# Performance work log

Hardware: AMD Instinct MI355X
Metric: run time of the kernel (lower is better)

The kernel has to match this reference:

```python
import jax, jax.numpy as jnp
import numpy as np

NUM_HEADS = 8
IN_DIM = 384
HEAD_DIM = IN_DIM // NUM_HEADS  # 48


def setup_inputs() -> dict:
    key = jax.random.key(0)
    ks = jax.random.split(key, 6)
    B, N, M, C = 4, 4096, 1024, 384
    q_x = jax.random.normal(ks[0], (B, N, C), dtype=jnp.float32)
    kv_x = jax.random.normal(ks[1], (B, M, C), dtype=jnp.float32)
    s = C ** -0.5  # fan-in style init scale
    Wq = jax.random.normal(ks[2], (C, IN_DIM), dtype=jnp.float32) * s
    Wkv = jax.random.normal(ks[3], (C, 2 * IN_DIM), dtype=jnp.float32) * s
    Wproj = jax.random.normal(ks[4], (IN_DIM, IN_DIM), dtype=jnp.float32) * (IN_DIM ** -0.5)
    bproj = jnp.zeros((IN_DIM,), dtype=jnp.float32)
    return {"q_x": q_x, "kv_x": kv_x, "Wq": Wq, "Wkv": Wkv, "Wproj": Wproj, "bproj": bproj}


def reference(q_x, kv_x, Wq, Wkv, Wproj, bproj):
    B, N, C = q_x.shape
    M = kv_x.shape[1]
    scale = HEAD_DIM ** -0.5
    # q: [B, H, N, hd]
    q = (q_x @ Wq).reshape(B, N, NUM_HEADS, HEAD_DIM).transpose(0, 2, 1, 3)
    # k, v: [B, H, M, hd]
    kv = (kv_x @ Wkv).reshape(B, M, 2, NUM_HEADS, HEAD_DIM).transpose(2, 0, 3, 1, 4)
    k, v = kv[0], kv[1]
    # attention scores [B, H, N, M]
    attn = jax.nn.softmax(jnp.einsum('bhnd,bhmd->bhnm', q, k) * scale, axis=-1)
    x = jnp.einsum('bhnm,bhmd->bhnd', attn, v)  # [B, H, N, hd]
    x = x.transpose(0, 2, 1, 3).reshape(B, N, IN_DIM)
    x = x @ Wproj + bproj
    # sr_ratio == 1 residual: add raw q projection back
    q_res = q.transpose(0, 2, 1, 3).reshape(B, N, IN_DIM)
    return q_res + x
```

## Files before the change

### kernel.cpp

```cpp
#include <hip/hip_runtime.h>
#include <hip/hip_bf16.h>
#include <math.h>

#define B_ 4
#define N_ 4096
#define M_ 1024
#define C_ 384
#define NH_ 8
#define HD_ 48

typedef float f32x4 __attribute__((ext_vector_type(4)));
typedef float f32x16 __attribute__((ext_vector_type(16)));
typedef short bf16x8 __attribute__((ext_vector_type(8)));

typedef __attribute__((address_space(3))) unsigned int lds_uint;
typedef const __attribute__((address_space(1))) unsigned int glob_uint;

__device__ __forceinline__ void gld_lds16(const void* g, void* l) {
    __builtin_amdgcn_global_load_lds((glob_uint*)g, (lds_uint*)l, 16, 0, 0);
}

__device__ __forceinline__ unsigned short f2bf(float x) {
    unsigned int u = __builtin_bit_cast(unsigned int, x);
    return (unsigned short)((u + 0x7FFFu + ((u >> 16) & 1u)) >> 16);
}
__device__ __forceinline__ float bf2f(unsigned short x) {
    return __builtin_bit_cast(float, (unsigned int)x << 16);
}
__device__ __forceinline__ float fast_exp2(float x) {
#if __has_builtin(__builtin_amdgcn_exp2f)
    return __builtin_amdgcn_exp2f(x);
#else
    return exp2f(x);
#endif
}
__device__ __forceinline__ uint2 pack4_rne(float a, float b, float c, float d) {
    uint2 r;
    r.x = (unsigned int)f2bf(a) | ((unsigned int)f2bf(b) << 16);
    r.y = (unsigned int)f2bf(c) | ((unsigned int)f2bf(d) << 16);
    return r;
}

#define QSCALE 0.20823490983597203f
#define INV_QSCALE (1.0f / 0.20823490983597203f)

__global__ __launch_bounds__(256)
void prep(const float* __restrict__ qx_f, unsigned short* __restrict__ qx_bf,
          const float* __restrict__ kvx_f, unsigned short* __restrict__ kvx_bf,
          const float* __restrict__ Wq, const float* __restrict__ Wkv,
          const float* __restrict__ Wproj,
          unsigned short* __restrict__ Wq_t, unsigned short* __restrict__ Wkv_t,
          unsigned short* __restrict__ Wproj_t)
{
    __shared__ unsigned short T[64 * 72];
    const int tid = threadIdx.x;
    int bid = blockIdx.x;

    if (bid < 7680) {
        size_t i4 = (size_t)bid * 256 + tid;
        const float* src; unsigned short* dst;
        if (i4 < 1572864u) { src = qx_f; dst = qx_bf; }
        else { src = kvx_f; dst = kvx_bf; i4 -= 1572864u; }
        float4 v = *(const float4*)&src[i4 * 4];
        *(uint2*)&dst[i4 * 4] = pack4_rne(v.x, v.y, v.z, v.w);
        return;
    }

    bid -= 7680;
    const float* W; unsigned short* Wt; int N, kt, nt;
    if (bid < 36)       { W = Wq;    Wt = Wq_t;    N = 384; kt = bid / 6;  nt = bid - kt * 6; }
    else if (bid < 108) { bid -= 36;  W = Wkv;   Wt = Wkv_t;   N = 768; kt = bid / 12; nt = bid - kt * 12; }
    else                { bid -= 108; W = Wproj; Wt = Wproj_t; N = 384; kt = bid / 6;  nt = bid - kt * 6; }
    const int k0 = kt * 64, n0 = nt * 64;

    #pragma unroll
    for (int it = 0; it < 4; ++it) {
        int k = it * 16 + (tid >> 4);
        int n4 = (tid & 15) * 4;
        float4 v = *(const float4*)&W[(size_t)(k0 + k) * N + n0 + n4];
        T[(n4 + 0) * 72 + k] = f2bf(v.x);
        T[(n4 + 1) * 72 + k] = f2bf(v.y);
        T[(n4 + 2) * 72 + k] = f2bf(v.z);
        T[(n4 + 3) * 72 + k] = f2bf(v.w);
    }
    __syncthreads();
    #pragma unroll
    for (int i = 0; i < 2; ++i) {
        int s = tid + 256 * i;
        int n = s >> 3, part = s & 7;
        *(uint4*)&Wt[(size_t)(n0 + n) * C_ + k0 + part * 8] = *(const uint4*)&T[n * 72 + part * 8];
    }
}

__device__ __forceinline__ void stage128(const unsigned short* src, unsigned short* lds,
                                         int kk, int tid) {
    #pragma unroll
    for (int r = 0; r < 4; ++r) {
        int off = r * 256 + tid;
        int row = off >> 3;
        int c = off & 7;
        int gc = c ^ (row & 7);
        gld_lds16(src + (size_t)row * C_ + kk + gc * 8, lds + (size_t)off * 8);
    }
}
__device__ __forceinline__ void stage64(const unsigned short* src, unsigned short* lds,
                                        int kk, int tid) {
    #pragma unroll
    for (int r = 0; r < 2; ++r) {
        int off = r * 256 + tid;
        int row = off >> 3;
        int c = off & 7;
        int gc = c ^ (row & 7);
        gld_lds16(src + (size_t)row * C_ + kk + gc * 8, lds + (size_t)off * 8);
    }
}
__device__ __forceinline__ bf16x8 frag_ld(const unsigned short* lds, int row, int chunk) {
    return *(const bf16x8*)&lds[row * 64 + ((chunk ^ (row & 7)) << 3)];
}

#define GEMM_CORE(Aptr, Wptr)                                                        \
    f32x4 acc[4][4];                                                                 \
    _Pragma("unroll")                                                                \
    for (int rt = 0; rt < 4; ++rt)                                                   \
        _Pragma("unroll")                                                            \
        for (int ct = 0; ct < 4; ++ct) acc[rt][ct] = (f32x4){0.f, 0.f, 0.f, 0.f};    \
    const int wrow0 = (wave & 1) * 64;                                               \
    const int wcol0 = (wave >> 1) * 64;                                              \
    for (int kk = 0; kk < C_; kk += 64) {                                            \
        __syncthreads();                                                             \
        stage128(Aptr, As, kk, tid);                                                 \
        stage128(Wptr, Ws, kk, tid);                                                 \
        __syncthreads();                                                             \
        _Pragma("unroll")                                                            \
        for (int ks = 0; ks < 2; ++ks) {                                             \
            bf16x8 af[4], wf[4];                                                     \
            _Pragma("unroll")                                                        \
            for (int rt = 0; rt < 4; ++rt)                                           \
                af[rt] = frag_ld(As, wrow0 + rt * 16 + ln, ks * 4 + quad);           \
            _Pragma("unroll")                                                        \
            for (int ct = 0; ct < 4; ++ct)                                           \
                wf[ct] = frag_ld(Ws, wcol0 + ct * 16 + ln, ks * 4 + quad);           \
            _Pragma("unroll")                                                        \
            for (int rt = 0; rt < 4; ++rt)                                           \
                _Pragma("unroll")                                                    \
                for (int ct = 0; ct < 4; ++ct)                                       \
                    acc[rt][ct] = __builtin_amdgcn_mfma_f32_16x16x32_bf16(           \
                        wf[ct], af[rt], acc[rt][ct], 0, 0, 0);                       \
        }                                                                            \
    }

__global__ __launch_bounds__(256)
void gemm_qkv(const unsigned short* __restrict__ qx, const unsigned short* __restrict__ kvx,
              const unsigned short* __restrict__ Wqt, const unsigned short* __restrict__ Wkvt,
              unsigned short* __restrict__ qbf,
              unsigned short* __restrict__ kbf, unsigned short* __restrict__ vbf)
{
    __shared__ unsigned short As[128 * 64];
    __shared__ unsigned short Ws[128 * 64];
    const int tid = threadIdx.x;
    const int wave = tid >> 6;
    const int lane = tid & 63;
    const int ln = lane & 15;
    const int quad = lane >> 4;

    int bid = blockIdx.x;
    int mode, row0, col0;
    const unsigned short *A, *Wt;
    if (bid < 384) { mode = 0; A = qx;  Wt = Wqt;  row0 = (bid / 3) * 128; col0 = (bid % 3) * 128; }
    else { bid -= 384; mode = 1; A = kvx; Wt = Wkvt; row0 = (bid / 6) * 128; col0 = (bid % 6) * 128; }

    GEMM_CORE(A + (size_t)row0 * C_, Wt + (size_t)col0 * C_)

    #pragma unroll
    for (int rt = 0; rt < 4; ++rt) {
        int grow = row0 + wrow0 + rt * 16 + ln;
        #pragma unroll
        for (int ct = 0; ct < 4; ++ct) {
            int col = col0 + wcol0 + ct * 16 + quad * 4;
            f32x4 v = acc[rt][ct];
            if (mode == 0) {
                int b = grow >> 12, n = grow & (N_ - 1);
                int h = col / HD_, d = col - h * HD_;
                *(uint2*)&qbf[(((size_t)(b * NH_ + h) * N_) + n) * HD_ + d] =
                    pack4_rne(v[0] * QSCALE, v[1] * QSCALE, v[2] * QSCALE, v[3] * QSCALE);
            } else {
                int b = grow >> 10, m = grow & (M_ - 1);
                if (col < C_) {
                    int h = col / HD_, d = col - h * HD_;
                    *(uint2*)&kbf[(((size_t)(b * NH_ + h) * M_) + m) * HD_ + d] =
                        pack4_rne(v[0], v[1], v[2], v[3]);
                } else {
                    int c2 = col - C_;
                    int h = c2 / HD_, d = c2 - h * HD_;
                    size_t base = ((size_t)(b * NH_ + h) * HD_ + d) * M_ + m;
                    #pragma unroll
                    for (int r = 0; r < 4; ++r) vbf[base + (size_t)r * M_] = f2bf(v[r]);
                }
            }
        }
    }
}

__global__ __launch_bounds__(256)
void gemm_out(const unsigned short* __restrict__ A, const unsigned short* __restrict__ Wt,
              float* __restrict__ out0,
              const unsigned short* __restrict__ qbf, const float* __restrict__ bias)
{
    __shared__ unsigned short As[128 * 64];
    __shared__ unsigned short Ws[64 * 64];
    const int tid = threadIdx.x;
    const int wave = tid >> 6;
    const int lane = tid & 63;
    const int ln = lane & 15;
    const int quad = lane >> 4;
    const int row0 = (blockIdx.x / 6) * 128;
    const int col0 = (blockIdx.x % 6) * 64;
    const int wrow0 = (wave & 1) * 64;
    const int wcol0 = (wave >> 1) * 32;

    f32x4 acc[4][2];
    #pragma unroll
    for (int rt = 0; rt < 4; ++rt)
        #pragma unroll
        for (int ct = 0; ct < 2; ++ct) acc[rt][ct] = (f32x4){0.f, 0.f, 0.f, 0.f};

    const unsigned short* Ap = A + (size_t)row0 * C_;
    const unsigned short* Wp = Wt + (size_t)col0 * C_;
    for (int kk = 0; kk < C_; kk += 64) {
        __syncthreads();
        stage128(Ap, As, kk, tid);
        stage64(Wp, Ws, kk, tid);
        __syncthreads();
        #pragma unroll
        for (int ks = 0; ks < 2; ++ks) {
            bf16x8 af[4], wf[2];
            #pragma unroll
            for (int rt = 0; rt < 4; ++rt)
                af[rt] = frag_ld(As, wrow0 + rt * 16 + ln, ks * 4 + quad);
            #pragma unroll
            for (int ct = 0; ct < 2; ++ct)
                wf[ct] = frag_ld(Ws, wcol0 + ct * 16 + ln, ks * 4 + quad);
            #pragma unroll
            for (int rt = 0; rt < 4; ++rt)
                #pragma unroll
                for (int ct = 0; ct < 2; ++ct)
                    acc[rt][ct] = __builtin_amdgcn_mfma_f32_16x16x32_bf16(
                        wf[ct], af[rt], acc[rt][ct], 0, 0, 0);
        }
    }

    #pragma unroll
    for (int rt = 0; rt < 4; ++rt) {
        int grow = row0 + wrow0 + rt * 16 + ln;
        #pragma unroll
        for (int ct = 0; ct < 2; ++ct) {
            int col = col0 + wcol0 + ct * 16 + quad * 4;
            f32x4 v = acc[rt][ct];
            size_t idx = (size_t)grow * C_ + col;
            int b = grow >> 12, n = grow & (N_ - 1);
            int h = col / HD_, d = col - h * HD_;
            uint2 ad = *(const uint2*)&qbf[(((size_t)(b * NH_ + h) * N_) + n) * HD_ + d];
            float4 bi = *(const float4*)&bias[col];
            float4 o;
            o.x = v[0] + bf2f((unsigned short)(ad.x & 0xFFFF)) * INV_QSCALE + bi.x;
            o.y = v[1] + bf2f((unsigned short)(ad.x >> 16))    * INV_QSCALE + bi.y;
            o.z = v[2] + bf2f((unsigned short)(ad.y & 0xFFFF)) * INV_QSCALE + bi.z;
            o.w = v[3] + bf2f((unsigned short)(ad.y >> 16))    * INV_QSCALE + bi.w;
            *(float4*)&out0[idx] = o;
        }
    }
}

__device__ __forceinline__ void attn_load(bf16x8 (&ka)[3], bf16x8 (&va)[2][2],
                                          const unsigned short* kb,
                                          const unsigned short* vb,
                                          int m0, int l31, int hi)
{
    #pragma unroll
    for (int s = 0; s < 3; ++s)
        ka[s] = *(const bf16x8*)&kb[(size_t)(m0 + l31) * HD_ + s * 16 + hi * 8];
    #pragma unroll
    for (int ot2 = 0; ot2 < 2; ++ot2)
        #pragma unroll
        for (int s2 = 0; s2 < 2; ++s2)
            va[ot2][s2] = *(const bf16x8*)&vb[(size_t)(ot2 * 32 + l31) * M_ + m0 + s2 * 16 + hi * 8];
}

__device__ __forceinline__ void attn_compute(const bf16x8 (&ka)[3], const bf16x8 (&va)[2][2],
                                             const bf16x8 (&qb)[2][3],
                                             f32x16 (&O)[2][2], float (&rs)[2], int hi)
{
    #pragma unroll
    for (int qt = 0; qt < 2; ++qt) {
        f32x16 S;
        #pragma unroll
        for (int r = 0; r < 16; ++r) S[r] = 0.f;
        __builtin_amdgcn_s_setprio(1);
        #pragma unroll
        for (int s = 0; s < 3; ++s)
            S = __builtin_amdgcn_mfma_f32_32x32x16_bf16(ka[s], qb[qt][s], S, 0, 0, 0);
        __builtin_amdgcn_s_setprio(0);

        float p[16];
        #pragma unroll
        for (int r = 0; r < 16; ++r) p[r] = fast_exp2(S[r]);
        {
            float s0 = (p[0] + p[1]) + (p[2] + p[3]);
            float s1 = (p[4] + p[5]) + (p[6] + p[7]);
            float s2 = (p[8] + p[9]) + (p[10] + p[11]);
            float s3 = (p[12] + p[13]) + (p[14] + p[15]);
            rs[qt] += (s0 + s1) + (s2 + s3);
        }

        unsigned c0[4], c1[4];
        #pragma unroll
        for (int g = 0; g < 4; ++g) {
            c0[g] = (__builtin_bit_cast(unsigned int, p[4 * g + 0]) >> 16) |
                    (__builtin_bit_cast(unsigned int, p[4 * g + 1]) & 0xFFFF0000u);
            c1[g] = (__builtin_bit_cast(unsigned int, p[4 * g + 2]) >> 16) |
                    (__builtin_bit_cast(unsigned int, p[4 * g + 3]) & 0xFFFF0000u);
        }

        #pragma unroll
        for (int s2 = 0; s2 < 2; ++s2) {
            unsigned o00 = c0[2 * s2], o01 = c0[2 * s2 + 1];
            unsigned o10 = c1[2 * s2], o11 = c1[2 * s2 + 1];
            unsigned pr0 = (unsigned)__shfl_xor((int)(hi ? o00 : o01), 32);
            unsigned pr1 = (unsigned)__shfl_xor((int)(hi ? o10 : o11), 32);
            unsigned d0 = hi ? pr0 : o00;
            unsigned d1 = hi ? pr1 : o10;
            unsigned d2 = hi ? o01 : pr0;
            unsigned d3 = hi ? o11 : pr1;
            uint4 u = {d0, d1, d2, d3};
            bf16x8 pf = __builtin_bit_cast(bf16x8, u);
            __builtin_amdgcn_s_setprio(1);
            #pragma unroll
            for (int ot2 = 0; ot2 < 2; ++ot2)
                O[qt][ot2] = __builtin_amdgcn_mfma_f32_32x32x16_bf16(
                    va[ot2][s2], pf, O[qt][ot2], 0, 0, 0);
            __builtin_amdgcn_s_setprio(0);
        }
    }
}

__global__ __launch_bounds__(256, 2)
void attn_mfma(const unsigned short* __restrict__ qbf,
               const unsigned short* __restrict__ kbf,
               const unsigned short* __restrict__ vbf,
               unsigned short* __restrict__ of)
{
    const int tid = threadIdx.x;
    const int wave = tid >> 6;
    const int lane = tid & 63;
    const int l31 = lane & 31;
    const int hi  = lane >> 5;
    const int bh = blockIdx.x;
    const int n0w = blockIdx.y * 256 + wave * 64;

    const unsigned short* kb = kbf + (size_t)bh * M_ * HD_;
    const unsigned short* vb = vbf + (size_t)bh * HD_ * M_;

    bf16x8 qb[2][3];
    #pragma unroll
    for (int qt = 0; qt < 2; ++qt) {
        const unsigned short* qp = qbf + ((size_t)bh * N_ + n0w + qt * 32 + l31) * HD_;
        #pragma unroll
        for (int s = 0; s < 3; ++s)
            qb[qt][s] = *(const bf16x8*)(qp + s * 16 + hi * 8);
    }

    f32x16 O[2][2];
    #pragma unroll
    for (int qt = 0; qt < 2; ++qt)
        #pragma unroll
        for (int ot2 = 0; ot2 < 2; ++ot2)
            #pragma unroll
            for (int r = 0; r < 16; ++r) O[qt][ot2][r] = 0.f;
    float rs[2] = {0.f, 0.f};

    bf16x8 kaA[3], vaA[2][2], kaB[3], vaB[2][2];
    attn_load(kaA, vaA, kb, vb, 0, l31, hi);

    for (int mtt = 0; mtt < 32; mtt += 2) {
        attn_load(kaB, vaB, kb, vb, (mtt + 1) * 32, l31, hi);
        attn_compute(kaA, vaA, qb, O, rs, hi);
        if (mtt + 2 < 32)
            attn_load(kaA, vaA, kb, vb, (mtt + 2) * 32, l31, hi);
        attn_compute(kaB, vaB, qb, O, rs, hi);
    }

    float inv[2];
    #pragma unroll
    for (int qt = 0; qt < 2; ++qt) {
        float x = rs[qt] + __shfl_xor(rs[qt], 32);
        inv[qt] = 1.0f / x;
    }

    const int b = bh >> 3, h = bh & 7;
    #pragma unroll
    for (int qt = 0; qt < 2; ++qt) {
        size_t grow = (size_t)b * N_ + n0w + qt * 32 + l31;
        unsigned short* orow = of + grow * C_ + h * HD_;
        #pragma unroll
        for (int ot2 = 0; ot2 < 2; ++ot2) {
            const int rgmax = (ot2 == 0) ? 4 : 2;
            #pragma unroll
            for (int rg = 0; rg < 4; ++rg) {
                if (rg >= rgmax) continue;
                int d0 = ot2 * 32 + rg * 8 + hi * 4;
                *(uint2*)(orow + d0) = pack4_rne(
                    O[qt][ot2][rg * 4 + 0] * inv[qt], O[qt][ot2][rg * 4 + 1] * inv[qt],
                    O[qt][ot2][rg * 4 + 2] * inv[qt], O[qt][ot2][rg * 4 + 3] * inv[qt]);
            }
        }
    }
}

extern "C" void kernel_launch(void* const* d_in, const int* in_sizes, int n_in,
                              void* d_out, int out_size, void* d_ws, size_t ws_size,
                              hipStream_t stream) {
    const float* q_x   = (const float*)d_in[0];
    const float* kv_x  = (const float*)d_in[1];
    const float* Wq    = (const float*)d_in[2];
    const float* Wkv   = (const float*)d_in[3];
    const float* Wproj = (const float*)d_in[4];
    const float* bproj = (const float*)d_in[5];
    float* out = (float*)d_out;

    unsigned short* qbf     = (unsigned short*)d_ws;
    unsigned short* kbf     = qbf     + 6291456;
    unsigned short* vbf     = kbf     + 1572864;
    unsigned short* of      = vbf     + 1572864;
    unsigned short* qx_bf   = of      + 6291456;
    unsigned short* kvx_bf  = qx_bf   + 6291456;
    unsigned short* Wq_t    = kvx_bf  + 1572864;
    unsigned short* Wkv_t   = Wq_t    + 147456;
    unsigned short* Wproj_t = Wkv_t   + 294912;

    dim3 blk(256);

    prep<<<dim3(7824), blk, 0, stream>>>(q_x, qx_bf, kv_x, kvx_bf,
                                         Wq, Wkv, Wproj, Wq_t, Wkv_t, Wproj_t);

    gemm_qkv<<<dim3(576), blk, 0, stream>>>(
        qx_bf, kvx_bf, Wq_t, Wkv_t, qbf, kbf, vbf);

    attn_mfma<<<dim3(32, 16), blk, 0, stream>>>(qbf, kbf, vbf, of);

    gemm_out<<<dim3(768), blk, 0, stream>>>(of, Wproj_t, out, qbf, bproj);
}
```

Baseline: 168.6 us.

## Fuse all stages into one cooperative persistent kernel with grid syncs

Replaces the four kernel launches (prep, QKV GEMM, attention, output GEMM) with a single cooperative kernel of 512 blocks that loops over work units and uses grid.sync between stages, keeping the old multi-kernel path as a fallback if cooperative launch fails. It also removes the double-buffered register prefetch and setprio hints in the attention loop, loading K/V fragments inline. This aims to cut launch overhead and inter-kernel gaps, but it limits each stage to 512 resident blocks, so the GEMM stages get uneven tail work. The fused kernel also carries the attention register pressure and the 2-blocks-per-CU launch bound into every stage.

Measured after the change: 390.9 us. +131.8%, slower.

```diff
diff --git a/kernel.cpp b/kernel.cpp
--- a/kernel.cpp
+++ b/kernel.cpp
@@ -1,6 +1,9 @@
 #include <hip/hip_runtime.h>
+#include <hip/hip_cooperative_groups.h>
 #include <hip/hip_bf16.h>
 #include <math.h>
+
+namespace cg = cooperative_groups;
 
 #define B_ 4
 #define N_ 4096
@@ -44,54 +47,6 @@
 #define QSCALE 0.20823490983597203f
 #define INV_QSCALE (1.0f / 0.20823490983597203f)
 
-__global__ __launch_bounds__(256)
-void prep(const float* __restrict__ qx_f, unsigned short* __restrict__ qx_bf,
-          const float* __restrict__ kvx_f, unsigned short* __restrict__ kvx_bf,
-          const float* __restrict__ Wq, const float* __restrict__ Wkv,
-          const float* __restrict__ Wproj,
-          unsigned short* __restrict__ Wq_t, unsigned short* __restrict__ Wkv_t,
-          unsigned short* __restrict__ Wproj_t)
-{
-    __shared__ unsigned short T[64 * 72];
-    const int tid = threadIdx.x;
-    int bid = blockIdx.x;
-
-    if (bid < 7680) {
-        size_t i4 = (size_t)bid * 256 + tid;
-        const float* src; unsigned short* dst;
-        if (i4 < 1572864u) { src = qx_f; dst = qx_bf; }
-        else { src = kvx_f; dst = kvx_bf; i4 -= 1572864u; }
-        float4 v = *(const float4*)&src[i4 * 4];
-        *(uint2*)&dst[i4 * 4] = pack4_rne(v.x, v.y, v.z, v.w);
-        return;
-    }
-
-    bid -= 7680;
-    const float* W; unsigned short* Wt; int N, kt, nt;
-    if (bid < 36)       { W = Wq;    Wt = Wq_t;    N = 384; kt = bid / 6;  nt = bid - kt * 6; }
-    else if (bid < 108) { bid -= 36;  W = Wkv;   Wt = Wkv_t;   N = 768; kt = bid / 12; nt = bid - kt * 12; }
-    else                { bid -= 108; W = Wproj; Wt = Wproj_t; N = 384; kt = bid / 6;  nt = bid - kt * 6; }
-    const int k0 = kt * 64, n0 = nt * 64;
-
-    #pragma unroll
-    for (int it = 0; it < 4; ++it) {
-        int k = it * 16 + (tid >> 4);
-        int n4 = (tid & 15) * 4;
-        float4 v = *(const float4*)&W[(size_t)(k0 + k) * N + n0 + n4];
-        T[(n4 + 0) * 72 + k] = f2bf(v.x);
-        T[(n4 + 1) * 72 + k] = f2bf(v.y);
-        T[(n4 + 2) * 72 + k] = f2bf(v.z);
-        T[(n4 + 3) * 72 + k] = f2bf(v.w);
-    }
-    __syncthreads();
-    #pragma unroll
-    for (int i = 0; i < 2; ++i) {
-        int s = tid + 256 * i;
-        int n = s >> 3, part = s & 7;
-        *(uint4*)&Wt[(size_t)(n0 + n) * C_ + k0 + part * 8] = *(const uint4*)&T[n * 72 + part * 8];
-    }
-}
-
 __device__ __forceinline__ void stage128(const unsigned short* src, unsigned short* lds,
                                          int kk, int tid) {
     #pragma unroll
@@ -116,6 +71,48 @@
 }
 __device__ __forceinline__ bf16x8 frag_ld(const unsigned short* lds, int row, int chunk) {
     return *(const bf16x8*)&lds[row * 64 + ((chunk ^ (row & 7)) << 3)];
+}
+
+__device__ __forceinline__ void prep_unit(
+    int u, const float* q_x, const float* kv_x,
+    const float* Wq, const float* Wkv, const float* Wproj,
+    unsigned short* qx_bf, unsigned short* kvx_bf,
+    unsigned short* Wq_t, unsigned short* Wkv_t, unsigned short* Wproj_t,
+    unsigned short* T, int tid)
+{
+    if (u < 7680) {
+        size_t i4 = (size_t)u * 256 + tid;
+        const float* src; unsigned short* dst;
+        if (i4 < 1572864u) { src = q_x; dst = qx_bf; }
+        else { src = kv_x; dst = kvx_bf; i4 -= 1572864u; }
+        float4 v = *(const float4*)&src[i4 * 4];
+        *(uint2*)&dst[i4 * 4] = pack4_rne(v.x, v.y, v.z, v.w);
+        return;
+    }
+    int wb = u - 7680;
+    const float* W; unsigned short* Wt; int Nn, kt, nt;
+    if (wb < 36)       { W = Wq;    Wt = Wq_t;    Nn = 384; kt = wb / 6;  nt = wb - kt * 6; }
+    else if (wb < 108) { wb -= 36;  W = Wkv;   Wt = Wkv_t;   Nn = 768; kt = wb / 12; nt = wb - kt * 12; }
+    else               { wb -= 108; W = Wproj; Wt = Wproj_t; Nn = 384; kt = wb / 6;  nt = wb - kt * 6; }
+    const int k0 = kt * 64, n0 = nt * 64;
+
+    #pragma unroll
+    for (int it = 0; it < 4; ++it) {
+        int k = it * 16 + (tid >> 4);
+        int n4 = (tid & 15) * 4;
+        float4 v = *(const float4*)&W[(size_t)(k0 + k) * Nn + n0 + n4];
+        T[(n4 + 0) * 72 + k] = f2bf(v.x);
+        T[(n4 + 1) * 72 + k] = f2bf(v.y);
+        T[(n4 + 2) * 72 + k] = f2bf(v.z);
+        T[(n4 + 3) * 72 + k] = f2bf(v.w);
+    }
+    __syncthreads();
+    #pragma unroll
+    for (int i = 0; i < 2; ++i) {
+        int s = tid + 256 * i;
+        int n = s >> 3, part = s & 7;
+        *(uint4*)&Wt[(size_t)(n0 + n) * C_ + k0 + part * 8] = *(const uint4*)&T[n * 72 + part * 8];
+    }
 }
 
 #define GEMM_CORE(Aptr, Wptr)                                                        \
@@ -149,25 +146,21 @@
         }                                                                            \
     }
 
-__global__ __launch_bounds__(256)
-void gemm_qkv(const unsigned short* __restrict__ qx, const unsigned short* __restrict__ kvx,
-              const unsigned short* __restrict__ Wqt, const unsigned short* __restrict__ Wkvt,
-              unsigned short* __restrict__ qbf,
-              unsigned short* __restrict__ kbf, unsigned short* __restrict__ vbf)
-{
-    __shared__ unsigned short As[128 * 64];
-    __shared__ unsigned short Ws[128 * 64];
-    const int tid = threadIdx.x;
+__device__ __forceinline__ void qkv_tile(
+    int t, const unsigned short* qx, const unsigned short* kvx,
+    const unsigned short* Wqt, const unsigned short* Wkvt,
+    unsigned short* qbf, unsigned short* kbf, unsigned short* vbf,
+    unsigned short* As, unsigned short* Ws, int tid)
+{
     const int wave = tid >> 6;
     const int lane = tid & 63;
     const int ln = lane & 15;
     const int quad = lane >> 4;
-
-    int bid = blockIdx.x;
+    int bb = t;
     int mode, row0, col0;
     const unsigned short *A, *Wt;
-    if (bid < 384) { mode = 0; A = qx;  Wt = Wqt;  row0 = (bid / 3) * 128; col0 = (bid % 3) * 128; }
-    else { bid -= 384; mode = 1; A = kvx; Wt = Wkvt; row0 = (bid / 6) * 128; col0 = (bid % 6) * 128; }
+    if (bb < 384) { mode = 0; A = qx;  Wt = Wqt;  row0 = (bb / 3) * 128; col0 = (bb % 3) * 128; }
+    else { bb -= 384; mode = 1; A = kvx; Wt = Wkvt; row0 = (bb / 6) * 128; col0 = (bb % 6) * 128; }
 
     GEMM_CORE(A + (size_t)row0 * C_, Wt + (size_t)col0 * C_)
 
@@ -201,20 +194,17 @@
     }
 }
 
-__global__ __launch_bounds__(256)
-void gemm_out(const unsigned short* __restrict__ A, const unsigned short* __restrict__ Wt,
-              float* __restrict__ out0,
-              const unsigned short* __restrict__ qbf, const float* __restrict__ bias)
-{
-    __shared__ unsigned short As[128 * 64];
-    __shared__ unsigned short Ws[64 * 64];
-    const int tid = threadIdx.x;
+__device__ __forceinline__ void out_tile(
+    int t, const unsigned short* A, const unsigned short* Wt, float* out0,
+    const unsigned short* qbf, const float* bias,
+    unsigned short* As, unsigned short* Ws, int tid)
+{
     const int wave = tid >> 6;
     const int lane = tid & 63;
     const int ln = lane & 15;
     const int quad = lane >> 4;
-    const int row0 = (blockIdx.x / 6) * 128;
-    const int col0 = (blockIdx.x % 6) * 64;
+    const int row0 = (t / 6) * 128;
+    const int col0 = (t % 6) * 64;
     const int wrow0 = (wave & 1) * 64;
     const int wcol0 = (wave >> 1) * 32;
 
@@ -271,91 +261,15 @@
     }
 }
 
-__device__ __forceinline__ void attn_load(bf16x8 (&ka)[3], bf16x8 (&va)[2][2],
-                                          const unsigned short* kb,
-                                          const unsigned short* vb,
-                                          int m0, int l31, int hi)
-{
-    #pragma unroll
-    for (int s = 0; s < 3; ++s)
-        ka[s] = *(const bf16x8*)&kb[(size_t)(m0 + l31) * HD_ + s * 16 + hi * 8];
-    #pragma unroll
-    for (int ot2 = 0; ot2 < 2; ++ot2)
-        #pragma unroll
-        for (int s2 = 0; s2 < 2; ++s2)
-            va[ot2][s2] = *(const bf16x8*)&vb[(size_t)(ot2 * 32 + l31) * M_ + m0 + s2 * 16 + hi * 8];
-}
-
-__device__ __forceinline__ void attn_compute(const bf16x8 (&ka)[3], const bf16x8 (&va)[2][2],
-                                             const bf16x8 (&qb)[2][3],
-                                             f32x16 (&O)[2][2], float (&rs)[2], int hi)
-{
-    #pragma unroll
-    for (int qt = 0; qt < 2; ++qt) {
-        f32x16 S;
-        #pragma unroll
-        for (int r = 0; r < 16; ++r) S[r] = 0.f;
-        __builtin_amdgcn_s_setprio(1);
-        #pragma unroll
-        for (int s = 0; s < 3; ++s)
-            S = __builtin_amdgcn_mfma_f32_32x32x16_bf16(ka[s], qb[qt][s], S, 0, 0, 0);
-        __builtin_amdgcn_s_setprio(0);
-
-        float p[16];
-        #pragma unroll
-        for (int r = 0; r < 16; ++r) p[r] = fast_exp2(S[r]);
-        {
-            float s0 = (p[0] + p[1]) + (p[2] + p[3]);
-            float s1 = (p[4] + p[5]) + (p[6] + p[7]);
-            float s2 = (p[8] + p[9]) + (p[10] + p[11]);
-            float s3 = (p[12] + p[13]) + (p[14] + p[15]);
-            rs[qt] += (s0 + s1) + (s2 + s3);
-        }
-
-        unsigned c0[4], c1[4];
-        #pragma unroll
-        for (int g = 0; g < 4; ++g) {
-            c0[g] = (__builtin_bit_cast(unsigned int, p[4 * g + 0]) >> 16) |
-                    (__builtin_bit_cast(unsigned int, p[4 * g + 1]) & 0xFFFF0000u);
-            c1[g] = (__builtin_bit_cast(unsigned int, p[4 * g + 2]) >> 16) |
-                    (__builtin_bit_cast(unsigned int, p[4 * g + 3]) & 0xFFFF0000u);
-        }
-
-        #pragma unroll
-        for (int s2 = 0; s2 < 2; ++s2) {
-            unsigned o00 = c0[2 * s2], o01 = c0[2 * s2 + 1];
-            unsigned o10 = c1[2 * s2], o11 = c1[2 * s2 + 1];
-            unsigned pr0 = (unsigned)__shfl_xor((int)(hi ? o00 : o01), 32);
-            unsigned pr1 = (unsigned)__shfl_xor((int)(hi ? o10 : o11), 32);
-            unsigned d0 = hi ? pr0 : o00;
-            unsigned d1 = hi ? pr1 : o10;
-            unsigned d2 = hi ? o01 : pr0;
-            unsigned d3 = hi ? o11 : pr1;
-            uint4 u = {d0, d1, d2, d3};
-            bf16x8 pf = __builtin_bit_cast(bf16x8, u);
-            __builtin_amdgcn_s_setprio(1);
-            #pragma unroll
-            for (int ot2 = 0; ot2 < 2; ++ot2)
-                O[qt][ot2] = __builtin_amdgcn_mfma_f32_32x32x16_bf16(
-                    va[ot2][s2], pf, O[qt][ot2], 0, 0, 0);
-            __builtin_amdgcn_s_setprio(0);
-        }
-    }
-}
-
-__global__ __launch_bounds__(256, 2)
-void attn_mfma(const unsigned short* __restrict__ qbf,
-               const unsigned short* __restrict__ kbf,
-               const unsigned short* __restrict__ vbf,
-               unsigned short* __restrict__ of)
-{
-    const int tid = threadIdx.x;
+__device__ __forceinline__ void attn_block(
+    int bh, int ny, const unsigned short* qbf, const unsigned short* kbf,
+    const unsigned short* vbf, unsigned short* of, int tid)
+{
     const int wave = tid >> 6;
     const int lane = tid & 63;
     const int l31 = lane & 31;
     const int hi  = lane >> 5;
-    const int bh = blockIdx.x;
-    const int n0w = blockIdx.y * 256 + wave * 64;
+    const int n0w = ny * 256 + wave * 64;
 
     const unsigned short* kb = kbf + (size_t)bh * M_ * HD_;
     const unsigned short* vb = vbf + (size_t)bh * HD_ * M_;
@@ -378,15 +292,68 @@
             for (int r = 0; r < 16; ++r) O[qt][ot2][r] = 0.f;
     float rs[2] = {0.f, 0.f};
 
-    bf16x8 kaA[3], vaA[2][2], kaB[3], vaB[2][2];
-    attn_load(kaA, vaA, kb, vb, 0, l31, hi);
-
-    for (int mtt = 0; mtt < 32; mtt += 2) {
-        attn_load(kaB, vaB, kb, vb, (mtt + 1) * 32, l31, hi);
-        attn_compute(kaA, vaA, qb, O, rs, hi);
-        if (mtt + 2 < 32)
-            attn_load(kaA, vaA, kb, vb, (mtt + 2) * 32, l31, hi);
-        attn_compute(kaB, vaB, qb, O, rs, hi);
+    for (int mtt = 0; mtt < 32; ++mtt) {
+        const int m0 = mtt * 32;
+
+        bf16x8 ka[3];
+        #pragma unroll
+        for (int s = 0; s < 3; ++s)
+            ka[s] = *(const bf16x8*)&kb[(size_t)(m0 + l31) * HD_ + s * 16 + hi * 8];
+
+        bf16x8 va[2][2];
+        #pragma unroll
+        for (int ot2 = 0; ot2 < 2; ++ot2)
+            #pragma unroll
+            for (int s2 = 0; s2 < 2; ++s2)
+                va[ot2][s2] = *(const bf16x8*)&vb[(size_t)(ot2 * 32 + l31) * M_ + m0 + s2 * 16 + hi * 8];
+
+        #pragma unroll
+        for (int qt = 0; qt < 2; ++qt) {
+            f32x16 S;
+            #pragma unroll
+            for (int r = 0; r < 16; ++r) S[r] = 0.f;
+            #pragma unroll
+            for (int s = 0; s < 3; ++s)
+                S = __builtin_amdgcn_mfma_f32_32x32x16_bf16(ka[s], qb[qt][s], S, 0, 0, 0);
+
+            float p[16];
+            #pragma unroll
+            for (int r = 0; r < 16; ++r) p[r] = fast_exp2(S[r]);
+            {
+                float s0 = (p[0] + p[1]) + (p[2] + p[3]);
+                float s1 = (p[4] + p[5]) + (p[6] + p[7]);
+                float s2 = (p[8] + p[9]) + (p[10] + p[11]);
+                float s3 = (p[12] + p[13]) + (p[14] + p[15]);
+                rs[qt] += (s0 + s1) + (s2 + s3);
+            }
+
+            unsigned c0[4], c1[4];
+            #pragma unroll
+            for (int g = 0; g < 4; ++g) {
+                c0[g] = (__builtin_bit_cast(unsigned int, p[4 * g + 0]) >> 16) |
+                        (__builtin_bit_cast(unsigned int, p[4 * g + 1]) & 0xFFFF0000u);
+                c1[g] = (__builtin_bit_cast(unsigned int, p[4 * g + 2]) >> 16) |
+                        (__builtin_bit_cast(unsigned int, p[4 * g + 3]) & 0xFFFF0000u);
+            }
+
+            #pragma unroll
+            for (int s2 = 0; s2 < 2; ++s2) {
+                unsigned o00 = c0[2 * s2], o01 = c0[2 * s2 + 1];
+                unsigned o10 = c1[2 * s2], o11 = c1[2 * s2 + 1];
+                unsigned pr0 = (unsigned)__shfl_xor((int)(hi ? o00 : o01), 32);
+                unsigned pr1 = (unsigned)__shfl_xor((int)(hi ? o10 : o11), 32);
+                unsigned d0 = hi ? pr0 : o00;
+                unsigned d1 = hi ? pr1 : o10;
+                unsigned d2 = hi ? o01 : pr0;
+                unsigned d3 = hi ? o11 : pr1;
+                uint4 u = {d0, d1, d2, d3};
+                bf16x8 pf = __builtin_bit_cast(bf16x8, u);
+                #pragma unroll
+                for (int ot2 = 0; ot2 < 2; ++ot2)
+                    O[qt][ot2] = __builtin_amdgcn_mfma_f32_32x32x16_bf16(
+                        va[ot2][s2], pf, O[qt][ot2], 0, 0, 0);
+            }
+        }
     }
 
     float inv[2];
@@ -414,6 +381,80 @@
             }
         }
     }
+}
+
+__global__ __launch_bounds__(256, 2)
+void fused(const float* __restrict__ q_x, const float* __restrict__ kv_x,
+           const float* __restrict__ Wq, const float* __restrict__ Wkv,
+           const float* __restrict__ Wproj, const float* __restrict__ bproj,
+           float* __restrict__ out,
+           unsigned short* __restrict__ qbf, unsigned short* __restrict__ kbf,
+           unsigned short* __restrict__ vbf, unsigned short* __restrict__ of,
+           unsigned short* __restrict__ qx_bf, unsigned short* __restrict__ kvx_bf,
+           unsigned short* __restrict__ Wq_t, unsigned short* __restrict__ Wkv_t,
+           unsigned short* __restrict__ Wproj_t)
+{
+    cg::grid_group grid = cg::this_grid();
+    __shared__ unsigned short As[128 * 64];
+    __shared__ unsigned short Ws[128 * 64];
+    const int tid = threadIdx.x;
+    const int bid0 = blockIdx.x;
+
+    for (int u = bid0; u < 7824; u += 512)
+        prep_unit(u, q_x, kv_x, Wq, Wkv, Wproj, qx_bf, kvx_bf,
+                  Wq_t, Wkv_t, Wproj_t, As, tid);
+    grid.sync();
+
+    for (int t = bid0; t < 576; t += 512)
+        qkv_tile(t, qx_bf, kvx_bf, Wq_t, Wkv_t, qbf, kbf, vbf, As, Ws, tid);
+    grid.sync();
+
+    attn_block(bid0 & 31, bid0 >> 5, qbf, kbf, vbf, of, tid);
+    grid.sync();
+
+    for (int t = bid0; t < 768; t += 512)
+        out_tile(t, of, Wproj_t, out, qbf, bproj, As, Ws, tid);
+}
+
+__global__ __launch_bounds__(256)
+void prep_k(const float* __restrict__ q_x, const float* __restrict__ kv_x,
+            const float* __restrict__ Wq, const float* __restrict__ Wkv,
+            const float* __restrict__ Wproj,
+            unsigned short* __restrict__ qx_bf, unsigned short* __restrict__ kvx_bf,
+            unsigned short* __restrict__ Wq_t, unsigned short* __restrict__ Wkv_t,
+            unsigned short* __restrict__ Wproj_t)
+{
+    __shared__ unsigned short T[128 * 64];
+    prep_unit(blockIdx.x, q_x, kv_x, Wq, Wkv, Wproj, qx_bf, kvx_bf,
+              Wq_t, Wkv_t, Wproj_t, T, threadIdx.x);
+}
+
+__global__ __launch_bounds__(256)
+void gemm_qkv_k(const unsigned short* __restrict__ qx, const unsigned short* __restrict__ kvx,
+                const unsigned short* __restrict__ Wqt, const unsigned short* __restrict__ Wkvt,
+                unsigned short* __restrict__ qbf,
+                unsigned short* __restrict__ kbf, unsigned short* __restrict__ vbf)
+{
+    __shared__ unsigned short As[128 * 64];
+    __shared__ unsigned short Ws[128 * 64];
+    qkv_tile(blockIdx.x, qx, kvx, Wqt, Wkvt, qbf, kbf, vbf, As, Ws, threadIdx.x);
+}
+
+__global__ __launch_bounds__(256, 2)
+void attn_k(const unsigned short* __restrict__ qbf, const unsigned short* __restrict__ kbf,
+            const unsigned short* __restrict__ vbf, unsigned short* __restrict__ of)
+{
+    attn_block(blockIdx.x, blockIdx.y, qbf, kbf, vbf, of, threadIdx.x);
+}
+
+__global__ __launch_bounds__(256)
+void gemm_out_k(const unsigned short* __restrict__ A, const unsigned short* __restrict__ Wt,
+                float* __restrict__ out0,
+                const unsigned short* __restrict__ qbf, const float* __restrict__ bias)
+{
+    __shared__ unsigned short As[128 * 64];
+    __shared__ unsigned short Ws[64 * 64];
+    out_tile(blockIdx.x, A, Wt, out0, qbf, bias, As, Ws, threadIdx.x);
 }
 
 extern "C" void kernel_launch(void* const* d_in, const int* in_sizes, int n_in,
@@ -437,15 +478,21 @@
     unsigned short* Wkv_t   = Wq_t    + 147456;
     unsigned short* Wproj_t = Wkv_t   + 294912;
 
-    dim3 blk(256);
-
-    prep<<<dim3(7824), blk, 0, stream>>>(q_x, qx_bf, kv_x, kvx_bf,
-                                         Wq, Wkv, Wproj, Wq_t, Wkv_t, Wproj_t);
-
-    gemm_qkv<<<dim3(576), blk, 0, stream>>>(
-        qx_bf, kvx_bf, Wq_t, Wkv_t, qbf, kbf, vbf);
-
-    attn_mfma<<<dim3(32, 16), blk, 0, stream>>>(qbf, kbf, vbf, of);
-
-    gemm_out<<<dim3(768), blk, 0, stream>>>(of, Wproj_t, out, qbf, bproj);
-}
+    void* args[] = {
+        (void*)&q_x, (void*)&kv_x, (void*)&Wq, (void*)&Wkv, (void*)&Wproj,
+        (void*)&bproj, (void*)&out, (void*)&qbf, (void*)&kbf, (void*)&vbf,
+        (void*)&of, (void*)&qx_bf, (void*)&kvx_bf, (void*)&Wq_t, (void*)&Wkv_t,
+        (void*)&Wproj_t
+    };
+    hipError_t e = hipLaunchCooperativeKernel((const void*)fused, dim3(512), dim3(256),
+                                              args, 0, stream);
+    if (e != hipSuccess) {
+        dim3 blk(256);
+        prep_k<<<dim3(7824), blk, 0, stream>>>(q_x, kv_x, Wq, Wkv, Wproj,
+                                               qx_bf, kvx_bf, Wq_t, Wkv_t, Wproj_t);
+        gemm_qkv_k<<<dim3(576), blk, 0, stream>>>(qx_bf, kvx_bf, Wq_t, Wkv_t,
+                                                  qbf, kbf, vbf);
+        attn_k<<<dim3(32, 16), blk, 0, stream>>>(qbf, kbf, vbf, of);
+        gemm_out_k<<<dim3(768), blk, 0, stream>>>(of, Wproj_t, out, qbf, bproj);
+    }
+}
```
